# Performance work log

Measured on AMD Instinct MI355X. Metric: run time of the kernel, lower is better.

The kernel has to match this reference:

```python
import jax, jax.numpy as jnp
import numpy as np

NEG_SLOPE = 0.2  # PyG GATConv default negative_slope


def _gat_conv(h_in, src, dst, W, a_src, a_dst, b, num_nodes, heads, out_dim, concat):
    # h: [N, heads, out_dim]
    h = (h_in @ W).reshape(num_nodes, heads, out_dim)
    # per-node attention contributions: [N, heads]
    alpha_s = jnp.einsum('nhd,hd->nh', h, a_src)
    alpha_d = jnp.einsum('nhd,hd->nh', h, a_dst)
    # per-edge logits: [E, heads]
    e = jax.nn.leaky_relu(alpha_s[src] + alpha_d[dst], NEG_SLOPE)
    # segment softmax over destination nodes
    m = jax.ops.segment_max(e, dst, num_segments=num_nodes)
    m = jnp.where(jnp.isfinite(m), m, 0.0)
    e = jnp.exp(e - m[dst])
    denom = jax.ops.segment_sum(e, dst, num_segments=num_nodes)
    alpha = e / (denom[dst] + 1e-16)  # [E, heads]
    # weighted scatter-aggregate of source features
    msg = h[src] * alpha[:, :, None]  # [E, heads, out_dim]
    out = jax.ops.segment_sum(msg, dst, num_segments=num_nodes)  # [N, heads, out_dim]
    if concat:
        out = out.reshape(num_nodes, heads * out_dim)
    else:
        out = out.mean(axis=1)
    return out + b


def setup_inputs() -> dict:
    key = jax.random.key(0)
    ks = jax.random.split(key, 9)
    N, E, IN, D, H = 50000, 800000, 256, 64, 4
    x = jax.random.normal(ks[0], (N, IN), dtype=jnp.float32)
    edge_index = jax.random.randint(ks[1], (2, E), 0, N, dtype=jnp.int32)
    s = 0.06  # small init scale
    W1 = jax.random.normal(ks[2], (IN, H * D), dtype=jnp.float32) * s
    att_src1 = jax.random.normal(ks[3], (H, D), dtype=jnp.float32) * s
    att_dst1 = jax.random.normal(ks[4], (H, D), dtype=jnp.float32) * s
    b1 = jnp.zeros((H * D,), dtype=jnp.float32)
    W2 = jax.random.normal(ks[5], (H * D, D), dtype=jnp.float32) * s
    att_src2 = jax.random.normal(ks[6], (1, D), dtype=jnp.float32) * s
    att_dst2 = jax.random.normal(ks[7], (1, D), dtype=jnp.float32) * s
    b2 = jnp.zeros((D,), dtype=jnp.float32)
    return {"x": x, "edge_index": edge_index, "W1": W1, "att_src1": att_src1,
            "att_dst1": att_dst1, "b1": b1, "W2": W2, "att_src2": att_src2,
            "att_dst2": att_dst2, "b2": b2}


def reference(x, edge_index, W1, att_src1, att_dst1, b1, W2, att_src2, att_dst2, b2):
    N = x.shape[0]
    H, D = att_src1.shape
    # PyG GATConv adds self-loops by default
    loop = jnp.arange(N, dtype=edge_index.dtype)
    src = jnp.concatenate([edge_index[0], loop])
    dst = jnp.concatenate([edge_index[1], loop])
    h = _gat_conv(x, src, dst, W1, att_src1, att_dst1, b1, N, H, D, concat=True)
    h = jax.nn.relu(h)  # dropout is eval no-op
    out = _gat_conv(h, src, dst, W2, att_src2, att_dst2, b2, N, 1, D, concat=False)
    return out
```

## Files before the change

### kernel.cpp

```cpp
#include <hip/hip_runtime.h>
#include <hip/hip_bf16.h>

typedef __attribute__((ext_vector_type(8))) short short8v;
typedef __attribute__((ext_vector_type(4))) float f32x4;
typedef __attribute__((ext_vector_type(2))) float f32x2;

__device__ __forceinline__ float lrelu(float x) { return x > 0.f ? x : 0.2f * x; }
__device__ __forceinline__ ushort f2bf(float v) {
  __hip_bfloat16 b = __float2bfloat16(v);
  return *(ushort*)&b;
}
__device__ __forceinline__ float bf2f(ushort u) {
  return __uint_as_float(((unsigned)u) << 16);
}
__device__ __forceinline__ f32x2 unpk_lo_hi(unsigned u) {
  return (f32x2){__uint_as_float(u << 16), __uint_as_float(u & 0xFFFF0000u)};
}
__device__ __forceinline__ float cvtub0(unsigned u) {
  float f; asm("v_cvt_f32_ubyte0 %0, %1" : "=v"(f) : "v"(u)); return f;
}
__device__ __forceinline__ float cvtub1(unsigned u) {
  float f; asm("v_cvt_f32_ubyte1 %0, %1" : "=v"(f) : "v"(u)); return f;
}
__device__ __forceinline__ float cvtub2(unsigned u) {
  float f; asm("v_cvt_f32_ubyte2 %0, %1" : "=v"(f) : "v"(u)); return f;
}
__device__ __forceinline__ float cvtub3(unsigned u) {
  float f; asm("v_cvt_f32_ubyte3 %0, %1" : "=v"(f) : "v"(u)); return f;
}
__device__ __forceinline__ void gload16(const ushort* g, ushort* l) {
  __builtin_amdgcn_global_load_lds((const __attribute__((address_space(1))) void*)g,
                                   (__attribute__((address_space(3))) void*)l, 16, 0, 0);
}

__global__ __launch_bounds__(256) void prep_kernel(const float* __restrict__ x,
    const float* __restrict__ W1, const float* __restrict__ W2,
    const int* __restrict__ dst, ushort* __restrict__ A1, ushort* __restrict__ B1t,
    ushort* __restrict__ B2t, int* __restrict__ counts, ushort* __restrict__ rank,
    int N, int Mpad, int E, int Etot, int PX, int PW) {
  int b = blockIdx.x, t = threadIdx.x;
  if (b < PX) {
    int idx = (b * 256 + t) * 4;
    int row = idx >> 8, c = idx & 255;
    float4 v = (row < N) ? *(const float4*)&x[idx] : make_float4(0.f, 0.f, 0.f, 0.f);
    *(ushort4*)&A1[(size_t)row * 256 + c] =
        make_ushort4(f2bf(v.x), f2bf(v.y), f2bf(v.z), f2bf(v.w));
  } else if (b < PX + PW) {
    int idx = (b - PX) * 256 + t;
    if (idx < 256 * 256) {
      int k = idx >> 8, col = idx & 255;
      float v = W1[idx];
      ushort hi = f2bf(v), lo = f2bf(v - bf2f(hi));
      size_t bb = (size_t)col * 512;
      B1t[bb + k] = hi;
      B1t[bb + 256 + k] = lo;
    } else if (idx < 256 * 256 + 256 * 64) {
      int j = idx - 256 * 256;
      int k = j >> 6, col = j & 63;
      float v = W2[j];
      ushort hi = f2bf(v), lo = f2bf(v - bf2f(hi));
      size_t bb = (size_t)col * 512;
      B2t[bb + k] = hi;
      B2t[bb + 256 + k] = lo;
    }
  } else {
    int e = (b - PX - PW) * 256 + t;
    if (e < Etot) {
      int d = (e < E) ? dst[e] : (e - E);
      int r = atomicAdd(&counts[d], 1);
      rank[e] = (ushort)r;
    }
  }
}

template<int BN, int NF, int EPI, int KT, int KAT>
__global__ __launch_bounds__(256) void gemm_mfma(
    const ushort* __restrict__ A, const ushort* __restrict__ Bt,
    const float* __restrict__ avs, const float* __restrict__ avd,
    void* __restrict__ Hb, float* __restrict__ hs,
    float* __restrict__ os, float* __restrict__ od, int M, int NN) {
  constexpr int BM = 128, BK = 64;
  __shared__ ushort As[BM * BK];
  __shared__ ushort Bs[BN * BK];
  const int t = threadIdx.x, l = t & 63, w = t >> 6;
  const int l15 = l & 15, l4 = l >> 4;
  const int m0 = blockIdx.y * BM, n0 = blockIdx.x * BN;
  const int wr = w >> 1, wc = w & 1;
  f32x4 acc[4][NF];
#pragma unroll
  for (int m = 0; m < 4; ++m)
#pragma unroll
    for (int n = 0; n < NF; ++n) acc[m][n] = (f32x4){0.f, 0.f, 0.f, 0.f};

  for (int kk = 0; kk < KT; kk += BK) {
    const int ka = (kk < KAT) ? kk : kk - KAT;
    __syncthreads();
#pragma unroll
    for (int i = 0; i < 4; ++i) {
      int q = w * 4 + i;
      int c = q * 64 + l;
      int row = c >> 3, k8 = c & 7;
      int k8s = k8 ^ (row & 7);
      gload16(&A[(size_t)(m0 + row) * KAT + ka + k8s * 8], &As[q * 512]);
    }
    constexpr int BCHW = (BN * 8 / 64) / 4;
#pragma unroll
    for (int i = 0; i < BCHW; ++i) {
      int q = w * BCHW + i;
      int c = q * 64 + l;
      int col = c >> 3, k8 = c & 7;
      int k8s = k8 ^ (col & 7);
      gload16(&Bt[(size_t)(n0 + col) * KT + kk + k8s * 8], &Bs[q * 512]);
    }
    __syncthreads();
#pragma unroll
    for (int ks = 0; ks < 2; ++ks) {
      int kb = ks * 4 + l4;
      short8v af[4], bfr[NF];
#pragma unroll
      for (int m = 0; m < 4; ++m) {
        int row = wr * 64 + m * 16 + l15;
        af[m] = *(const short8v*)&As[row * 64 + (kb ^ (row & 7)) * 8];
      }
#pragma unroll
      for (int n = 0; n < NF; ++n) {
        int col = wc * (NF * 16) + n * 16 + l15;
        bfr[n] = *(const short8v*)&Bs[col * 64 + (kb ^ (col & 7)) * 8];
      }
#pragma unroll
      for (int m = 0; m < 4; ++m)
#pragma unroll
        for (int n = 0; n < NF; ++n)
          acc[m][n] = __builtin_amdgcn_mfma_f32_16x16x32_bf16(af[m], bfr[n], acc[m][n], 0, 0, 0);
    }
  }
  if (EPI == 1) {
    unsigned char* hq = (unsigned char*)Hb;
    const int head = (n0 + wc * 64) >> 6;
#pragma unroll
    for (int m = 0; m < 4; ++m) {
#pragma unroll
      for (int r = 0; r < 4; ++r) {
        int row = m0 + wr * 64 + m * 16 + l4 * 4 + r;
        float s = 0.f;
#pragma unroll
        for (int n = 0; n < NF; ++n) s = fmaxf(s, fabsf(acc[m][n][r]));
#pragma unroll
        for (int off = 1; off < 16; off <<= 1) s = fmaxf(s, __shfl_xor(s, off, 64));
        float inv = s > 0.f ? 127.f / s : 0.f;
        if (row < M) {
          unsigned char* rp = hq + (size_t)row * 256;
#pragma unroll
          for (int n = 0; n < NF; ++n) {
            int f = n * 16 + l15;
            int qv = (int)rintf(acc[m][n][r] * inv) + 128;
            rp[4 * f + head] = (unsigned char)qv;
          }
          if (l15 == 0) hs[(size_t)row * 4 + head] = s * (1.f / 127.f);
        }
      }
    }
  } else {
    ushort* hb = (ushort*)Hb;
#pragma unroll
    for (int m = 0; m < 4; ++m) {
      int rbase = m0 + wr * 64 + m * 16 + l4 * 4;
#pragma unroll
      for (int n = 0; n < NF; ++n) {
        int gcol = n0 + wc * (NF * 16) + n * 16 + l15;
#pragma unroll
        for (int r = 0; r < 4; ++r) {
          int row = rbase + r;
          if (row < M) hb[(size_t)row * NN + gcol] = f2bf(acc[m][n][r]);
        }
      }
    }
  }
  float cs[NF], cd[NF];
#pragma unroll
  for (int n = 0; n < NF; ++n) {
    int gc = n0 + wc * (NF * 16) + n * 16 + l15;
    cs[n] = avs[gc];
    cd[n] = avd[gc];
  }
  const int H = NN >> 6;
  const int head = (n0 + wc * (NF * 16)) >> 6;
#pragma unroll
  for (int m = 0; m < 4; ++m) {
#pragma unroll
    for (int r = 0; r < 4; ++r) {
      float ps = 0.f, pd = 0.f;
#pragma unroll
      for (int n = 0; n < NF; ++n) { ps += acc[m][n][r] * cs[n]; pd += acc[m][n][r] * cd[n]; }
#pragma unroll
      for (int off = 1; off < 16; off <<= 1) {
        ps += __shfl_xor(ps, off, 64);
        pd += __shfl_xor(pd, off, 64);
      }
      if (l15 == 0) {
        int row = m0 + wr * 64 + m * 16 + l4 * 4 + r;
        if (row < M) {
          if (NF == 4) {
            os[(size_t)row * H + head] = ps;
            od[(size_t)row * H + head] = pd;
          } else {
            atomicAdd(&os[row], ps);
            atomicAdd(&od[row], pd);
          }
        }
      }
    }
  }
}

static constexpr int SCB = 2048;

__global__ __launch_bounds__(256) void scan1_kernel(const int* __restrict__ counts,
    int* __restrict__ offsets, int* __restrict__ bsums, int n) {
  __shared__ int wsum[4];
  int t = threadIdx.x, lane = t & 63, w = t >> 6;
  int base = blockIdx.x * SCB + t * 8;
  int c[8];
  if (base + 7 < n) {
    int4 v0 = *(const int4*)&counts[base];
    int4 v1 = *(const int4*)&counts[base + 4];
    c[0] = v0.x; c[1] = v0.y; c[2] = v0.z; c[3] = v0.w;
    c[4] = v1.x; c[5] = v1.y; c[6] = v1.z; c[7] = v1.w;
  } else {
#pragma unroll
    for (int j = 0; j < 8; ++j) c[j] = (base + j < n) ? counts[base + j] : 0;
  }
  int ts = 0;
#pragma unroll
  for (int j = 0; j < 8; ++j) ts += c[j];
  int x = ts;
#pragma unroll
  for (int off = 1; off < 64; off <<= 1) {
    int y = __shfl_up(x, off, 64);
    if (lane >= off) x += y;
  }
  if (lane == 63) wsum[w] = x;
  __syncthreads();
  int wpre = 0;
  for (int ww = 0; ww < w; ++ww) wpre += wsum[ww];
  int ex = wpre + x - ts;
  int o[8];
#pragma unroll
  for (int j = 0; j < 8; ++j) { o[j] = ex; ex += c[j]; }
  if (base + 7 < n) {
    *(int4*)&offsets[base] = make_int4(o[0], o[1], o[2], o[3]);
    *(int4*)&offsets[base + 4] = make_int4(o[4], o[5], o[6], o[7]);
  } else {
#pragma unroll
    for (int j = 0; j < 8; ++j) if (base + j < n) offsets[base + j] = o[j];
  }
  if (t == 255) bsums[blockIdx.x] = wpre + x;
}

__global__ __launch_bounds__(256) void scan2_kernel(const int* __restrict__ bsums,
    int* __restrict__ bbase, int nb) {
  __shared__ int wsum[4];
  int t = threadIdx.x, lane = t & 63, w = t >> 6;
  int v = (t < nb) ? bsums[t] : 0;
  int x = v;
#pragma unroll
  for (int off = 1; off < 64; off <<= 1) {
    int y = __shfl_up(x, off, 64);
    if (lane >= off) x += y;
  }
  if (lane == 63) wsum[w] = x;
  __syncthreads();
  int wpre = 0;
  for (int ww = 0; ww < w; ++ww) wpre += wsum[ww];
  if (t < nb) bbase[t] = wpre + x - v;
}

__global__ __launch_bounds__(256) void scan3_kernel(int* __restrict__ offsets,
    const int* __restrict__ bbase, int n, int total) {
  int t = threadIdx.x;
  int bb = bbase[blockIdx.x];
  int base = blockIdx.x * SCB + t * 8;
  if (base + 7 < n) {
    int4 v0 = *(const int4*)&offsets[base];
    int4 v1 = *(const int4*)&offsets[base + 4];
    v0.x += bb; v0.y += bb; v0.z += bb; v0.w += bb;
    v1.x += bb; v1.y += bb; v1.z += bb; v1.w += bb;
    *(int4*)&offsets[base] = v0;
    *(int4*)&offsets[base + 4] = v1;
  } else {
#pragma unroll
    for (int j = 0; j < 8; ++j)
      if (base + j < n) offsets[base + j] += bb;
  }
  if (blockIdx.x == 0 && t == 0) offsets[n] = total;
}

__global__ __launch_bounds__(256) void scatter_kernel(const int* __restrict__ src,
    const int* __restrict__ dst, const ushort* __restrict__ rank,
    const int* __restrict__ offsets, ushort* __restrict__ src_sorted, int E, int Etot) {
  int e0 = (blockIdx.x * 256 + threadIdx.x) * 4;
  if (e0 + 3 < E) {
    int4 s4 = *(const int4*)&src[e0];
    int4 d4 = *(const int4*)&dst[e0];
    ushort4 r4 = *(const ushort4*)&rank[e0];
    src_sorted[offsets[d4.x] + r4.x] = (ushort)s4.x;
    src_sorted[offsets[d4.y] + r4.y] = (ushort)s4.y;
    src_sorted[offsets[d4.z] + r4.z] = (ushort)s4.z;
    src_sorted[offsets[d4.w] + r4.w] = (ushort)s4.w;
  } else {
#pragma unroll
    for (int j = 0; j < 4; ++j) {
      int e = e0 + j;
      if (e >= Etot) break;
      int s = (e < E) ? src[e] : (e - E);
      int d = (e < E) ? dst[e] : (e - E);
      src_sorted[offsets[d] + rank[e]] = (ushort)s;
    }
  }
}

__global__ __launch_bounds__(256) void agg1_kernel(const unsigned char* __restrict__ h1q,
    const float* __restrict__ hs, const float* __restrict__ as1,
    const float* __restrict__ ad1, const int* __restrict__ offsets,
    const ushort* __restrict__ src_sorted, const float* __restrict__ b1,
    ushort* __restrict__ A2, int N, int Mpad) {
  __shared__ float4 pl[4][64];
  __shared__ alignas(16) unsigned sl[4][64];
  int wv = threadIdx.x >> 6;
  int wid = (blockIdx.x << 2) + wv;
  int lane = threadIdx.x & 63;
  if (wid >= Mpad) return;
  size_t ab = (size_t)wid * 256;
  if (wid >= N) {
#pragma unroll
    for (int i = 0; i < 4; ++i) A2[ab + i * 64 + lane] = 0;
    return;
  }
  float4 ah = *(const float4*)&ad1[(size_t)wid * 4];
  int st = offsets[wid], en = offsets[wid + 1];
  float acc0 = 0.f, acc1 = 0.f, acc2 = 0.f, acc3 = 0.f;
  float ds0 = 0.f, ds1 = 0.f, ds2 = 0.f, ds3 = 0.f;
  float ws0 = 0.f, ws1 = 0.f, ws2 = 0.f, ws3 = 0.f;
  const unsigned lo4 = (unsigned)lane * 4;
  for (int c = st; c < en; c += 64) {
    int mye = c + lane;
    float4 w4 = make_float4(0.f, 0.f, 0.f, 0.f);
    unsigned soff = 0;
    if (mye < en) {
      int smy = (int)src_sorted[mye];
      soff = ((unsigned)smy << 8) + lo4;
      float4 a4 = *(const float4*)&as1[(size_t)smy * 4];
      float4 sc4 = *(const float4*)&hs[(size_t)smy * 4];
      float p0 = __expf(lrelu(a4.x + ah.x));
      float p1 = __expf(lrelu(a4.y + ah.y));
      float p2 = __expf(lrelu(a4.z + ah.z));
      float p3 = __expf(lrelu(a4.w + ah.w));
      ds0 += p0; ds1 += p1; ds2 += p2; ds3 += p3;
      w4 = make_float4(p0 * sc4.x, p1 * sc4.y, p2 * sc4.z, p3 * sc4.w);
      ws0 += w4.x; ws1 += w4.y; ws2 += w4.z; ws3 += w4.w;
    }
    pl[wv][lane] = w4;
    sl[wv][lane] = soff - lo4;
    int cnt = min(64, en - c);
    int e = 0;
    for (; e + 4 <= cnt; e += 4) {
      uint4 s4 = *(const uint4*)&sl[wv][e];
      float4 w0 = pl[wv][e + 0];
      float4 w1 = pl[wv][e + 1];
      float4 w2 = pl[wv][e + 2];
      float4 w3 = pl[wv][e + 3];
      unsigned u0 = *(const unsigned*)(h1q + (s4.x + lo4));
      unsigned u1 = *(const unsigned*)(h1q + (s4.y + lo4));
      unsigned u2 = *(const unsigned*)(h1q + (s4.z + lo4));
      unsigned u3 = *(const unsigned*)(h1q + (s4.w + lo4));
      acc0 = fmaf(w0.x, cvtub0(u0), acc0); acc1 = fmaf(w0.y, cvtub1(u0), acc1);
      acc2 = fmaf(w0.z, cvtub2(u0), acc2); acc3 = fmaf(w0.w, cvtub3(u0), acc3);
      acc0 = fmaf(w1.x, cvtub0(u1), acc0); acc1 = fmaf(w1.y, cvtub1(u1), acc1);
      acc2 = fmaf(w1.z, cvtub2(u1), acc2); acc3 = fmaf(w1.w, cvtub3(u1), acc3);
      acc0 = fmaf(w2.x, cvtub0(u2), acc0); acc1 = fmaf(w2.y, cvtub1(u2), acc1);
      acc2 = fmaf(w2.z, cvtub2(u2), acc2); acc3 = fmaf(w2.w, cvtub3(u2), acc3);
      acc0 = fmaf(w3.x, cvtub0(u3), acc0); acc1 = fmaf(w3.y, cvtub1(u3), acc1);
      acc2 = fmaf(w3.z, cvtub2(u3), acc2); acc3 = fmaf(w3.w, cvtub3(u3), acc3);
    }
    for (; e < cnt; ++e) {
      unsigned sb = sl[wv][e];
      float4 w4e = pl[wv][e];
      unsigned u = *(const unsigned*)(h1q + (sb + lo4));
      acc0 = fmaf(w4e.x, cvtub0(u), acc0); acc1 = fmaf(w4e.y, cvtub1(u), acc1);
      acc2 = fmaf(w4e.z, cvtub2(u), acc2); acc3 = fmaf(w4e.w, cvtub3(u), acc3);
    }
  }
#pragma unroll
  for (int off = 32; off > 0; off >>= 1) {
    ds0 += __shfl_xor(ds0, off, 64);
    ds1 += __shfl_xor(ds1, off, 64);
    ds2 += __shfl_xor(ds2, off, 64);
    ds3 += __shfl_xor(ds3, off, 64);
    ws0 += __shfl_xor(ws0, off, 64);
    ws1 += __shfl_xor(ws1, off, 64);
    ws2 += __shfl_xor(ws2, off, 64);
    ws3 += __shfl_xor(ws3, off, 64);
  }
  float v[4];
  v[0] = fmaxf((acc0 - 128.f * ws0) / (ds0 + 1e-16f) + b1[lane], 0.f);
  v[1] = fmaxf((acc1 - 128.f * ws1) / (ds1 + 1e-16f) + b1[64 + lane], 0.f);
  v[2] = fmaxf((acc2 - 128.f * ws2) / (ds2 + 1e-16f) + b1[128 + lane], 0.f);
  v[3] = fmaxf((acc3 - 128.f * ws3) / (ds3 + 1e-16f) + b1[192 + lane], 0.f);
#pragma unroll
  for (int h = 0; h < 4; ++h) A2[ab + h * 64 + lane] = f2bf(v[h]);
}

__global__ __launch_bounds__(256) void agg2_kernel(const ushort* __restrict__ h2b,
    const float* __restrict__ as2, const float* __restrict__ ad2,
    const int* __restrict__ offsets, const ushort* __restrict__ src_sorted,
    const float* __restrict__ b2, float* __restrict__ out, int N) {
  __shared__ float pl[4][64];
  __shared__ alignas(16) int sl[4][64];
  int wv = threadIdx.x >> 6;
  int wid = (blockIdx.x << 2) + wv;
  int lane = threadIdx.x & 63;
  if (wid >= N) return;
  const int qtr = lane >> 4;
  const int fl = lane & 15;
  float ah = ad2[wid];
  int st = offsets[wid], en = offsets[wid + 1];
  f32x2 a01 = (f32x2){0.f, 0.f}, a23 = (f32x2){0.f, 0.f};
  float ds = 0.f;
  for (int c = st; c < en; c += 64) {
    int mye = c + lane;
    float p = 0.f;
    int smy = 0;
    if (mye < en) {
      smy = (int)src_sorted[mye];
      p = __expf(lrelu(as2[smy] + ah));
    }
    ds += p;
    pl[wv][lane] = p;
    sl[wv][lane] = smy;
    int cnt = min(64, en - c);
    for (int e = 0; e < cnt; e += 4) {
      int e2 = e + qtr;
      int row = sl[wv][e2];
      float q = pl[wv][e2];
      uint2 u = *(const uint2*)&h2b[(size_t)row * 64 + fl * 4];
      a01 += (f32x2){q, q} * unpk_lo_hi(u.x);
      a23 += (f32x2){q, q} * unpk_lo_hi(u.y);
    }
  }
#pragma unroll
  for (int off = 32; off > 0; off >>= 1) ds += __shfl_xor(ds, off, 64);
#pragma unroll
  for (int off = 16; off <= 32; off <<= 1) {
    a01.x += __shfl_xor(a01.x, off, 64);
    a01.y += __shfl_xor(a01.y, off, 64);
    a23.x += __shfl_xor(a23.x, off, 64);
    a23.y += __shfl_xor(a23.y, off, 64);
  }
  if (lane < 16) {
    float inv = 1.f / (ds + 1e-16f);
    float4 bb = *(const float4*)&b2[fl * 4];
    float4 o;
    o.x = a01.x * inv + bb.x;
    o.y = a01.y * inv + bb.y;
    o.z = a23.x * inv + bb.z;
    o.w = a23.y * inv + bb.w;
    *(float4*)&out[(size_t)wid * 64 + fl * 4] = o;
  }
}

extern "C" void kernel_launch(void* const* d_in, const int* in_sizes, int n_in,
                              void* d_out, int out_size, void* d_ws, size_t ws_size,
                              hipStream_t stream) {
  const float* x      = (const float*)d_in[0];
  const int*   ei     = (const int*)d_in[1];
  const float* W1     = (const float*)d_in[2];
  const float* a_src1 = (const float*)d_in[3];
  const float* a_dst1 = (const float*)d_in[4];
  const float* b1     = (const float*)d_in[5];
  const float* W2     = (const float*)d_in[6];
  const float* a_src2 = (const float*)d_in[7];
  const float* a_dst2 = (const float*)d_in[8];
  const float* b2     = (const float*)d_in[9];
  float* out = (float*)d_out;

  const int IN = 256, HD = 256, D2 = 64;
  const int N = in_sizes[0] / IN;
  const int E = in_sizes[1] / 2;
  const int Etot = E + N;
  const int Mpad = ((N + 127) / 128) * 128;
  const int* srcp = ei;
  const int* dstp = ei + E;

  uintptr_t base = (uintptr_t)d_ws;
  auto alloc_bytes = [&](size_t nbytes) -> void* {
    void* p = (void*)base;
    base += (nbytes + 255) & ~(size_t)255;
    return p;
  };
  ushort* A1        = (ushort*)alloc_bytes((size_t)Mpad * 256 * 2);
  ushort* A2        = (ushort*)alloc_bytes((size_t)Mpad * 256 * 2);
  unsigned char* h1q = (unsigned char*)alloc_bytes((size_t)N * 256);
  float* hs         = (float*)alloc_bytes((size_t)N * 4 * 4);
  ushort* h2b       = (ushort*)alloc_bytes((size_t)N * D2 * 2);
  ushort* B1t       = (ushort*)alloc_bytes((size_t)HD * 512 * 2);
  ushort* B2t       = (ushort*)alloc_bytes((size_t)D2 * 512 * 2);
  float* as1        = (float*)alloc_bytes((size_t)N * 4 * 4);
  float* ad1        = (float*)alloc_bytes((size_t)N * 4 * 4);
  float* as2        = (float*)alloc_bytes((size_t)N * 4);
  float* ad2        = (float*)alloc_bytes((size_t)N * 4);
  int* counts       = (int*)alloc_bytes((size_t)(N + 1) * 4);
  uintptr_t zero_end = base;
  int* offsets      = (int*)alloc_bytes((size_t)(N + 1) * 4);
  ushort* rank      = (ushort*)alloc_bytes((size_t)Etot * 2);
  ushort* src_sorted = (ushort*)alloc_bytes((size_t)Etot * 2);
  int* bsums        = (int*)alloc_bytes(256 * 4);
  int* bbase        = (int*)alloc_bytes(256 * 4);

  hipMemsetAsync((void*)as2, 0, zero_end - (uintptr_t)as2, stream);

  const int nwb  = (N + 3) / 4;
  const int nwbp = (Mpad + 3) / 4;
  const int neb  = (Etot + 255) / 256;
  const int nsb  = (N + SCB - 1) / SCB;
  const int PX = Mpad / 4;
  const int PW = (256 * 256 + 256 * 64) / 256;

  prep_kernel<<<PX + PW + neb, 256, 0, stream>>>(x, W1, W2, dstp, A1, B1t, B2t,
                                                 counts, rank, N, Mpad, E, Etot, PX, PW);
  scan1_kernel<<<nsb, 256, 0, stream>>>(counts, offsets, bsums, N);
  scan2_kernel<<<1, 256, 0, stream>>>(bsums, bbase, nsb);
  scan3_kernel<<<nsb, 256, 0, stream>>>(offsets, bbase, N, Etot);
  scatter_kernel<<<(Etot + 1023) / 1024, 256, 0, stream>>>(srcp, dstp, rank, offsets,
                                                           src_sorted, E, Etot);
  gemm_mfma<128, 4, 1, 512, 256><<<dim3(HD / 128, Mpad / 128), 256, 0, stream>>>(
      A1, B1t, a_src1, a_dst1, (void*)h1q, hs, as1, ad1, N, HD);
  agg1_kernel<<<nwbp, 256, 0, stream>>>(h1q, hs, as1, ad1, offsets, src_sorted, b1, A2, N, Mpad);
  gemm_mfma<64, 2, 0, 512, 256><<<dim3(D2 / 64, Mpad / 128), 256, 0, stream>>>(
      A2, B2t, a_src2, a_dst2, (void*)h2b, nullptr, as2, ad2, N, D2);
  agg2_kernel<<<nwb, 256, 0, stream>>>(h2b, as2, ad2, offsets, src_sorted, b2, out, N);
}
```

Baseline: 210.9 us.

## Fold edge scatter into first GEMM launch as extra blocks

Removes the standalone scatter kernel and runs its work as extra grid rows in the first GEMM launch. The scatter and the GEMM do not depend on each other, so they can overlap and one launch is saved. It also drops a redundant add and subtract of the lane offset in agg1. The cost is a larger GEMM grid and extra kernel parameters. Block scheduling could also interleave the scatter blocks poorly with the GEMM tiles.

```diff
diff --git a/kernel.cpp b/kernel.cpp
--- a/kernel.cpp
+++ b/kernel.cpp
@@ -73,12 +73,38 @@
   }
 }
 
-template<int BN, int NF, int EPI, int KT, int KAT>
+template<int BN, int NF, int EPI, int KT, int KAT, bool FS>
 __global__ __launch_bounds__(256) void gemm_mfma(
     const ushort* __restrict__ A, const ushort* __restrict__ Bt,
     const float* __restrict__ avs, const float* __restrict__ avd,
     void* __restrict__ Hb, float* __restrict__ hs,
-    float* __restrict__ os, float* __restrict__ od, int M, int NN) {
+    float* __restrict__ os, float* __restrict__ od, int M, int NN,
+    const int* __restrict__ sc_src, const int* __restrict__ sc_dst,
+    const ushort* __restrict__ sc_rank, const int* __restrict__ sc_off,
+    ushort* __restrict__ sc_out, int E, int Etot, int NY) {
+  if (FS && (int)blockIdx.y >= NY) {
+    int seg = ((int)blockIdx.y - NY) * (int)gridDim.x + (int)blockIdx.x;
+    int e0 = (seg * 256 + (int)threadIdx.x) * 4;
+    if (e0 + 3 < E) {
+      int4 s4 = *(const int4*)&sc_src[e0];
+      int4 d4 = *(const int4*)&sc_dst[e0];
+      ushort4 r4 = *(const ushort4*)&sc_rank[e0];
+      sc_out[sc_off[d4.x] + r4.x] = (ushort)s4.x;
+      sc_out[sc_off[d4.y] + r4.y] = (ushort)s4.y;
+      sc_out[sc_off[d4.z] + r4.z] = (ushort)s4.z;
+      sc_out[sc_off[d4.w] + r4.w] = (ushort)s4.w;
+    } else {
+#pragma unroll
+      for (int j = 0; j < 4; ++j) {
+        int e = e0 + j;
+        if (e >= Etot) break;
+        int s = (e < E) ? sc_src[e] : (e - E);
+        int d = (e < E) ? sc_dst[e] : (e - E);
+        sc_out[sc_off[d] + sc_rank[e]] = (ushort)s;
+      }
+    }
+    return;
+  }
   constexpr int BM = 128, BK = 64;
   __shared__ ushort As[BM * BK];
   __shared__ ushort Bs[BN * BK];
@@ -295,30 +321,6 @@
   if (blockIdx.x == 0 && t == 0) offsets[n] = total;
 }
 
-__global__ __launch_bounds__(256) void scatter_kernel(const int* __restrict__ src,
-    const int* __restrict__ dst, const ushort* __restrict__ rank,
-    const int* __restrict__ offsets, ushort* __restrict__ src_sorted, int E, int Etot) {
-  int e0 = (blockIdx.x * 256 + threadIdx.x) * 4;
-  if (e0 + 3 < E) {
-    int4 s4 = *(const int4*)&src[e0];
-    int4 d4 = *(const int4*)&dst[e0];
-    ushort4 r4 = *(const ushort4*)&rank[e0];
-    src_sorted[offsets[d4.x] + r4.x] = (ushort)s4.x;
-    src_sorted[offsets[d4.y] + r4.y] = (ushort)s4.y;
-    src_sorted[offsets[d4.z] + r4.z] = (ushort)s4.z;
-    src_sorted[offsets[d4.w] + r4.w] = (ushort)s4.w;
-  } else {
-#pragma unroll
-    for (int j = 0; j < 4; ++j) {
-      int e = e0 + j;
-      if (e >= Etot) break;
-      int s = (e < E) ? src[e] : (e - E);
-      int d = (e < E) ? dst[e] : (e - E);
-      src_sorted[offsets[d] + rank[e]] = (ushort)s;
-    }
-  }
-}
-
 __global__ __launch_bounds__(256) void agg1_kernel(const unsigned char* __restrict__ h1q,
     const float* __restrict__ hs, const float* __restrict__ as1,
     const float* __restrict__ ad1, const int* __restrict__ offsets,
@@ -348,7 +350,7 @@
     unsigned soff = 0;
     if (mye < en) {
       int smy = (int)src_sorted[mye];
-      soff = ((unsigned)smy << 8) + lo4;
+      soff = ((unsigned)smy << 8);
       float4 a4 = *(const float4*)&as1[(size_t)smy * 4];
       float4 sc4 = *(const float4*)&hs[(size_t)smy * 4];
       float p0 = __expf(lrelu(a4.x + ah.x));
@@ -360,7 +362,7 @@
       ws0 += w4.x; ws1 += w4.y; ws2 += w4.z; ws3 += w4.w;
     }
     pl[wv][lane] = w4;
-    sl[wv][lane] = soff - lo4;
+    sl[wv][lane] = soff;
     int cnt = min(64, en - c);
     int e = 0;
     for (; e + 4 <= cnt; e += 4) {
@@ -524,18 +526,21 @@
   const int nsb  = (N + SCB - 1) / SCB;
   const int PX = Mpad / 4;
   const int PW = (256 * 256 + 256 * 64) / 256;
+  const int NY1 = Mpad / 128;
+  const int SB  = (Etot + 1023) / 1024;
+  const int SY  = (SB + 1) / 2;
 
   prep_kernel<<<PX + PW + neb, 256, 0, stream>>>(x, W1, W2, dstp, A1, B1t, B2t,
                                                  counts, rank, N, Mpad, E, Etot, PX, PW);
   scan1_kernel<<<nsb, 256, 0, stream>>>(counts, offsets, bsums, N);
   scan2_kernel<<<1, 256, 0, stream>>>(bsums, bbase, nsb);
   scan3_kernel<<<nsb, 256, 0, stream>>>(offsets, bbase, N, Etot);
-  scatter_kernel<<<(Etot + 1023) / 1024, 256, 0, stream>>>(srcp, dstp, rank, offsets,
-                                                           src_sorted, E, Etot);
-  gemm_mfma<128, 4, 1, 512, 256><<<dim3(HD / 128, Mpad / 128), 256, 0, stream>>>(
-      A1, B1t, a_src1, a_dst1, (void*)h1q, hs, as1, ad1, N, HD);
+  gemm_mfma<128, 4, 1, 512, 256, true><<<dim3(HD / 128, NY1 + SY), 256, 0, stream>>>(
+      A1, B1t, a_src1, a_dst1, (void*)h1q, hs, as1, ad1, N, HD,
+      srcp, dstp, rank, offsets, src_sorted, E, Etot, NY1);
   agg1_kernel<<<nwbp, 256, 0, stream>>>(h1q, hs, as1, ad1, offsets, src_sorted, b1, A2, N, Mpad);
-  gemm_mfma<64, 2, 0, 512, 256><<<dim3(D2 / 64, Mpad / 128), 256, 0, stream>>>(
-      A2, B2t, a_src2, a_dst2, (void*)h2b, nullptr, as2, ad2, N, D2);
+  gemm_mfma<64, 2, 0, 512, 256, false><<<dim3(D2 / 64, Mpad / 128), 256, 0, stream>>>(
+      A2, B2t, a_src2, a_dst2, (void*)h2b, nullptr, as2, ad2, N, D2,
+      nullptr, nullptr, nullptr, nullptr, nullptr, 0, 0, Mpad / 128);
   agg2_kernel<<<nwb, 256, 0, stream>>>(h2b, as2, ad2, offsets, src_sorted, b2, out, N);
 }
```

New measurement: 199.1 us. 5.6% less time.

## Fuse edge degree histogram into first GEMM launch as extra blocks

Applied to the files above, without the earlier changes.

The per-edge atomic degree counting and rank assignment moves out of the prep kernel into extra grid rows of the first MFMA GEMM. Those blocks handle four edges per thread with a vectorised dst load and ushort4 rank store. The atomic-heavy histogram now overlaps with the compute-bound GEMM, and the prep kernel only converts x and the weights. The agg1 source offset also drops a redundant add and subtract of the lane offset. The GEMM now runs before the CSR scan, and the extra blocks may add contention on the GEMM's compute units.

```diff
diff --git a/kernel.cpp b/kernel.cpp
--- a/kernel.cpp
+++ b/kernel.cpp
@@ -35,9 +35,8 @@
 
 __global__ __launch_bounds__(256) void prep_kernel(const float* __restrict__ x,
     const float* __restrict__ W1, const float* __restrict__ W2,
-    const int* __restrict__ dst, ushort* __restrict__ A1, ushort* __restrict__ B1t,
-    ushort* __restrict__ B2t, int* __restrict__ counts, ushort* __restrict__ rank,
-    int N, int Mpad, int E, int Etot, int PX, int PW) {
+    ushort* __restrict__ A1, ushort* __restrict__ B1t, ushort* __restrict__ B2t,
+    int N, int Mpad, int PX) {
   int b = blockIdx.x, t = threadIdx.x;
   if (b < PX) {
     int idx = (b * 256 + t) * 4;
@@ -45,7 +44,7 @@
     float4 v = (row < N) ? *(const float4*)&x[idx] : make_float4(0.f, 0.f, 0.f, 0.f);
     *(ushort4*)&A1[(size_t)row * 256 + c] =
         make_ushort4(f2bf(v.x), f2bf(v.y), f2bf(v.z), f2bf(v.w));
-  } else if (b < PX + PW) {
+  } else {
     int idx = (b - PX) * 256 + t;
     if (idx < 256 * 256) {
       int k = idx >> 8, col = idx & 255;
@@ -63,22 +62,39 @@
       B2t[bb + k] = hi;
       B2t[bb + 256 + k] = lo;
     }
-  } else {
-    int e = (b - PX - PW) * 256 + t;
-    if (e < Etot) {
-      int d = (e < E) ? dst[e] : (e - E);
-      int r = atomicAdd(&counts[d], 1);
-      rank[e] = (ushort)r;
-    }
-  }
-}
-
-template<int BN, int NF, int EPI, int KT, int KAT>
+  }
+}
+
+template<int BN, int NF, int EPI, int KT, int KAT, bool FH>
 __global__ __launch_bounds__(256) void gemm_mfma(
     const ushort* __restrict__ A, const ushort* __restrict__ Bt,
     const float* __restrict__ avs, const float* __restrict__ avd,
     void* __restrict__ Hb, float* __restrict__ hs,
-    float* __restrict__ os, float* __restrict__ od, int M, int NN) {
+    float* __restrict__ os, float* __restrict__ od, int M, int NN,
+    const int* __restrict__ h_dst, int* __restrict__ h_counts,
+    ushort* __restrict__ h_rank, int E, int Etot, int NY) {
+  if (FH && (int)blockIdx.y >= NY) {
+    int seg = ((int)blockIdx.y - NY) * (int)gridDim.x + (int)blockIdx.x;
+    int e0 = (seg * 256 + (int)threadIdx.x) * 4;
+    if (e0 + 3 < E) {
+      int4 d4 = *(const int4*)&h_dst[e0];
+      ushort4 r4;
+      r4.x = (ushort)atomicAdd(&h_counts[d4.x], 1);
+      r4.y = (ushort)atomicAdd(&h_counts[d4.y], 1);
+      r4.z = (ushort)atomicAdd(&h_counts[d4.z], 1);
+      r4.w = (ushort)atomicAdd(&h_counts[d4.w], 1);
+      *(ushort4*)&h_rank[e0] = r4;
+    } else {
+#pragma unroll
+      for (int j = 0; j < 4; ++j) {
+        int e = e0 + j;
+        if (e >= Etot) break;
+        int d = (e < E) ? h_dst[e] : (e - E);
+        h_rank[e] = (ushort)atomicAdd(&h_counts[d], 1);
+      }
+    }
+    return;
+  }
   constexpr int BM = 128, BK = 64;
   __shared__ ushort As[BM * BK];
   __shared__ ushort Bs[BN * BK];
@@ -348,7 +364,7 @@
     unsigned soff = 0;
     if (mye < en) {
       int smy = (int)src_sorted[mye];
-      soff = ((unsigned)smy << 8) + lo4;
+      soff = ((unsigned)smy << 8);
       float4 a4 = *(const float4*)&as1[(size_t)smy * 4];
       float4 sc4 = *(const float4*)&hs[(size_t)smy * 4];
       float p0 = __expf(lrelu(a4.x + ah.x));
@@ -360,7 +376,7 @@
       ws0 += w4.x; ws1 += w4.y; ws2 += w4.z; ws3 += w4.w;
     }
     pl[wv][lane] = w4;
-    sl[wv][lane] = soff - lo4;
+    sl[wv][lane] = soff;
     int cnt = min(64, en - c);
     int e = 0;
     for (; e + 4 <= cnt; e += 4) {
@@ -520,22 +536,25 @@
 
   const int nwb  = (N + 3) / 4;
   const int nwbp = (Mpad + 3) / 4;
-  const int neb  = (Etot + 255) / 256;
   const int nsb  = (N + SCB - 1) / SCB;
   const int PX = Mpad / 4;
   const int PW = (256 * 256 + 256 * 64) / 256;
-
-  prep_kernel<<<PX + PW + neb, 256, 0, stream>>>(x, W1, W2, dstp, A1, B1t, B2t,
-                                                 counts, rank, N, Mpad, E, Etot, PX, PW);
+  const int NY1 = Mpad / 128;
+  const int HB  = (Etot + 1023) / 1024;
+  const int HY  = (HB + 1) / 2;
+
+  prep_kernel<<<PX + PW, 256, 0, stream>>>(x, W1, W2, A1, B1t, B2t, N, Mpad, PX);
+  gemm_mfma<128, 4, 1, 512, 256, true><<<dim3(HD / 128, NY1 + HY), 256, 0, stream>>>(
+      A1, B1t, a_src1, a_dst1, (void*)h1q, hs, as1, ad1, N, HD,
+      dstp, counts, rank, E, Etot, NY1);
   scan1_kernel<<<nsb, 256, 0, stream>>>(counts, offsets, bsums, N);
   scan2_kernel<<<1, 256, 0, stream>>>(bsums, bbase, nsb);
   scan3_kernel<<<nsb, 256, 0, stream>>>(offsets, bbase, N, Etot);
   scatter_kernel<<<(Etot + 1023) / 1024, 256, 0, stream>>>(srcp, dstp, rank, offsets,
                                                            src_sorted, E, Etot);
-  gemm_mfma<128, 4, 1, 512, 256><<<dim3(HD / 128, Mpad / 128), 256, 0, stream>>>(
-      A1, B1t, a_src1, a_dst1, (void*)h1q, hs, as1, ad1, N, HD);
   agg1_kernel<<<nwbp, 256, 0, stream>>>(h1q, hs, as1, ad1, offsets, src_sorted, b1, A2, N, Mpad);
-  gemm_mfma<64, 2, 0, 512, 256><<<dim3(D2 / 64, Mpad / 128), 256, 0, stream>>>(
-      A2, B2t, a_src2, a_dst2, (void*)h2b, nullptr, as2, ad2, N, D2);
+  gemm_mfma<64, 2, 0, 512, 256, false><<<dim3(D2 / 64, Mpad / 128), 256, 0, stream>>>(
+      A2, B2t, a_src2, a_dst2, (void*)h2b, nullptr, as2, ad2, N, D2,
+      nullptr, nullptr, nullptr, 0, 0, Mpad / 128);
   agg2_kernel<<<nwb, 256, 0, stream>>>(h2b, as2, ad2, offsets, src_sorted, b2, out, N);
 }
```

Result: faster. 200.2 us (-5.1%).
